# Performance work log

Measured on AMD Instinct MI355X. Metric: run time of the kernel, lower is better.

Reference implementation:

```python
import jax, jax.numpy as jnp
import numpy as np

PATCH = 9  # patch_size
EPS = 1e-12  # F.normalize eps


def _l2norm(x, axis):
    n = jnp.sqrt(jnp.sum(x * x, axis=axis, keepdims=True))
    return x / jnp.maximum(n, EPS)


def setup_inputs() -> dict:
    key = jax.random.key(0)
    k1, k2, k3 = jax.random.split(key, 3)
    feat_tar = jax.random.normal(k1, (16384, 512), dtype=jnp.float32)
    feat_refs = jax.random.normal(k2, (8, 512, 16384), dtype=jnp.float32)
    label_refs = jax.random.uniform(k3, (8, 32, 128, 128), dtype=jnp.float32)
    return {"feat_tar": feat_tar, "feat_refs": feat_refs, "label_refs": label_refs}


def reference(feat_tar, feat_refs, label_refs):
    num_ctx, num_labels, h, w = label_refs.shape
    num_feats = feat_tar.shape[1]
    P, pad = PATCH, PATCH // 2

    # feature_normalization=True: L2-normalize along feature dim
    feat_tar = _l2norm(feat_tar, axis=1)           # [h*w, C]
    feat_refs = _l2norm(feat_refs, axis=1)         # [nc, C, h*w]

    tar = feat_tar.T.reshape(num_feats, h, w)      # [C, h, w]
    refs = feat_refs.reshape(num_ctx, num_feats, h, w)
    refs_pad = jnp.pad(refs, ((0, 0), (0, 0), (pad, pad), (pad, pad)))

    # local correlation: corr[b, dy*P+dx, y, x] = sum_c refs_pad[b,c,y+dy,x+dx] * tar[c,y,x]
    # (matches F.unfold(refs, P, padding=pad) * tar -> sum over c)
    rows = []
    for dy in range(P):
        for dx in range(P):
            win = jax.lax.dynamic_slice(
                refs_pad, (0, 0, dy, dx), (num_ctx, num_feats, h, w))
            rows.append(jnp.einsum('bchw,chw->bhw', win, tar))
    corr = jnp.stack(rows, axis=1)                 # [nc, P*P, h, w]

    aff = corr.reshape(num_ctx, P * P, h * w).transpose(0, 2, 1)  # [nc, h*w, P*P]

    # affinity_normalization = Softmax(dim=-1)
    return jax.nn.softmax(aff, axis=-1)
```

## Files before the change

### kernel.cpp

```cpp
#include <hip/hip_runtime.h>
#include <hip/hip_bf16.h>

#define HW 128
#define NPIX 16384
#define CDEP 512
#define NB 8
#define QT 32

typedef __attribute__((ext_vector_type(8))) short short8;
typedef __attribute__((ext_vector_type(8))) __bf16 bf16x8;
typedef __attribute__((ext_vector_type(4))) float f32x4;

static __device__ inline bf16x8 asbf(short8 v) {
  union { short8 s; bf16x8 b; } u; u.s = v; return u.b;
}

static __device__ inline unsigned short f2bf(float x) {
  unsigned u = __float_as_uint(x);
  unsigned r = (u + 0x7fffu + ((u >> 16) & 1u)) >> 16;
  return (unsigned short)r;
}

__global__ __launch_bounds__(256) void k_norm_tar(const float* __restrict__ ft,
                                                  unsigned short* __restrict__ T) {
  int wave = threadIdx.x >> 6, lane = threadIdx.x & 63;
  int p = blockIdx.x * 4 + wave;
  const float* row = ft + (size_t)p * CDEP + lane * 8;
  float4 v0 = *(const float4*)(row);
  float4 v1 = *(const float4*)(row + 4);
  float s = v0.x*v0.x + v0.y*v0.y + v0.z*v0.z + v0.w*v0.w
          + v1.x*v1.x + v1.y*v1.y + v1.z*v1.z + v1.w*v1.w;
  #pragma unroll
  for (int off = 1; off < 64; off <<= 1) s += __shfl_xor(s, off);
  float sc = 1.0f / fmaxf(sqrtf(s), 1e-12f);
  float vv[8] = {v0.x, v0.y, v0.z, v0.w, v1.x, v1.y, v1.z, v1.w};
  short8 pk;
  #pragma unroll
  for (int i = 0; i < 8; ++i) pk[i] = (short)f2bf(vv[i] * sc);
  *(short8*)(T + (size_t)p * CDEP + lane * 8) = pk;
}

__global__ __launch_bounds__(256) void k_norm_refs(const float* __restrict__ fr,
                                                   unsigned short* __restrict__ R,
                                                   int b_offset) {
  __shared__ float lds[QT][CDEP + 1];
  __shared__ float psum[QT][8];
  __shared__ float inv[QT];
  int b = b_offset + blockIdx.z;
  int q0 = blockIdx.x * QT;
  const float* src = fr + (size_t)b * CDEP * NPIX;
  int t = threadIdx.x;

  int g = t & 7, cy = t >> 3;
  #pragma unroll
  for (int it = 0; it < 16; ++it) {
    int c = it * 32 + cy;
    float4 v = *(const float4*)(src + (size_t)c * NPIX + q0 + g * 4);
    lds[g*4 + 0][c] = v.x;
    lds[g*4 + 1][c] = v.y;
    lds[g*4 + 2][c] = v.z;
    lds[g*4 + 3][c] = v.w;
  }
  __syncthreads();

  int p = t & 31, part = t >> 5;
  float s = 0.f;
  #pragma unroll
  for (int j = 0; j < 64; ++j) { float v = lds[p][part*64 + j]; s += v * v; }
  psum[p][part] = s;
  __syncthreads();
  if (t < QT) {
    float a = 0.f;
    #pragma unroll
    for (int j = 0; j < 8; ++j) a += psum[t][j];
    inv[t] = 1.0f / fmaxf(sqrtf(a), 1e-12f);
  }
  __syncthreads();

  unsigned short* dst = R + ((size_t)blockIdx.z * NPIX + q0) * CDEP;
  #pragma unroll 4
  for (int j = 0; j < QT; ++j) {
    float sc = inv[j];
    unsigned lo = f2bf(lds[j][2*t]     * sc);
    unsigned hi = f2bf(lds[j][2*t + 1] * sc);
    *(unsigned*)(dst + (size_t)j * CDEP + 2*t) = lo | (hi << 16);
  }
}

__global__ __launch_bounds__(256, 2) void k_corr(const unsigned short* __restrict__ Tb,
                                                 const unsigned short* __restrict__ Rall,
                                                 float* __restrict__ out,
                                                 int b_offset) {
  __shared__ __align__(16) unsigned char ldsb[65536];
  const int t = threadIdx.x;
  const int lane = t & 63, wave = t >> 6;
  const int wy = wave >> 1, wx = wave & 1;
  const int bx = blockIdx.x, by = blockIdx.y, bz = blockIdx.z;
  const int b = b_offset + bz;
  const short* Rb = (const short*)Rall + (size_t)bz * NPIX * CDEP;
  const short* Tp = (const short*)Tb;

  const int mA = lane & 15, kg = lane >> 4;
  const int py = by*8 + wy*4 + (mA >> 2), px = bx*8 + wx*4 + (mA & 3);
  const short* arow = Tp + (size_t)(py * HW + px) * CDEP + kg * 8;
  short8 a[16];
  #pragma unroll
  for (int kk = 0; kk < 16; ++kk) a[kk] = *(const short8*)(arow + kk * 32);

  const int slot = t & 7, qbase = t >> 3;
  int goff[8]; unsigned gval = 0; int loff[8];
  #pragma unroll
  for (int r = 0; r < 8; ++r) {
    int q = r * 32 + qbase;
    int gy = by*8 - 4 + (q >> 4);
    int gx = bx*8 - 4 + (q & 15);
    bool v = ((unsigned)gy < (unsigned)HW) && ((unsigned)gx < (unsigned)HW);
    if (v) gval |= (1u << r);
    goff[r] = v ? ((gy * HW + gx) * CDEP + slot * 8) : 0;
    loff[r] = q * 128 + ((slot * 16) ^ ((q & 7) << 4));
  }

  int qn[9];
  #pragma unroll
  for (int tt = 0; tt < 9; ++tt) {
    int idx = tt * 16 + (lane & 15);
    int qly = wy*4 + idx / 12, qlx = wx*4 + idx % 12;
    qn[tt] = qly * 16 + qlx;
  }

  f32x4 acc[9];
  #pragma unroll
  for (int tt = 0; tt < 9; ++tt) acc[tt] = (f32x4){0.f, 0.f, 0.f, 0.f};

  short8 st[8];
  const short8 z8 = {0,0,0,0,0,0,0,0};

  #pragma unroll
  for (int r = 0; r < 8; ++r)
    st[r] = ((gval >> r) & 1) ? *(const short8*)(Rb + goff[r]) : z8;
  #pragma unroll
  for (int r = 0; r < 8; ++r)
    *(short8*)(ldsb + loff[r]) = st[r];
  __syncthreads();

  #pragma unroll
  for (int ch = 0; ch < 8; ++ch) {
    if (ch < 7) {
      const short* src = Rb + (ch + 1) * 64;
      #pragma unroll
      for (int r = 0; r < 8; ++r)
        st[r] = ((gval >> r) & 1) ? *(const short8*)(src + goff[r]) : z8;
    }
    const int bufb = (ch & 1) << 15;
    #pragma unroll
    for (int step = 0; step < 2; ++step) {
      short8 af = a[ch * 2 + step];
      #pragma unroll
      for (int tt = 0; tt < 9; ++tt) {
        int q = qn[tt];
        int off = bufb + q * 128 + (((step << 6) | (kg << 4)) ^ ((q & 7) << 4));
        short8 bf = *(const short8*)(ldsb + off);
        acc[tt] = __builtin_amdgcn_mfma_f32_16x16x32_bf16(asbf(af), asbf(bf), acc[tt], 0, 0, 0);
      }
    }
    if (ch < 7) {
      const int nbuf = ((ch + 1) & 1) << 15;
      #pragma unroll
      for (int r = 0; r < 8; ++r)
        *(short8*)(ldsb + nbuf + loff[r]) = st[r];
      __syncthreads();
    }
  }

  __syncthreads();

  const int SSTR = 148;
  float* S = (float*)ldsb + wave * 16 * SSTR;
  #pragma unroll
  for (int tt = 0; tt < 9; ++tt) {
    #pragma unroll
    for (int r = 0; r < 4; ++r)
      S[(kg * 4 + r) * SSTR + tt * 16 + (lane & 15)] = acc[tt][r];
  }
  __syncthreads();

  const int mrow = lane >> 2, s4 = lane & 3;
  const int myy = mrow >> 2, mxx = mrow & 3;
  const float* Srow = S + mrow * SSTR;
  float vals[21];
  float mx = -3.0e38f;
  #pragma unroll
  for (int i = 0; i < 21; ++i) {
    int j = s4 + 4 * i;
    if (j < 81) {
      int dy = j / 9, dx = j % 9;
      float v = Srow[(myy + dy) * 12 + (mxx + dx)];
      vals[i] = v;
      mx = fmaxf(mx, v);
    }
  }
  mx = fmaxf(mx, __shfl_xor(mx, 1));
  mx = fmaxf(mx, __shfl_xor(mx, 2));
  float sum = 0.f;
  #pragma unroll
  for (int i = 0; i < 21; ++i) {
    int j = s4 + 4 * i;
    if (j < 81) { float e = __expf(vals[i] - mx); vals[i] = e; sum += e; }
  }
  sum += __shfl_xor(sum, 1);
  sum += __shfl_xor(sum, 2);
  float rs = 1.0f / sum;
  const int pg = (by*8 + wy*4 + myy) * HW + (bx*8 + wx*4 + mxx);
  float* op = out + ((size_t)b * NPIX + pg) * 81;
  #pragma unroll
  for (int i = 0; i < 21; ++i) {
    int j = s4 + 4 * i;
    if (j < 81) op[j] = vals[i] * rs;
  }
}

extern "C" void kernel_launch(void* const* d_in, const int* in_sizes, int n_in,
                              void* d_out, int out_size, void* d_ws, size_t ws_size,
                              hipStream_t stream) {
  const float* ft = (const float*)d_in[0];
  const float* fr = (const float*)d_in[1];
  float* out = (float*)d_out;
  unsigned short* T = (unsigned short*)d_ws;
  unsigned short* R = T + (size_t)NPIX * CDEP;
  size_t needAll = ((size_t)NPIX * CDEP + (size_t)NB * NPIX * CDEP) * 2;

  k_norm_tar<<<dim3(NPIX / 4), dim3(256), 0, stream>>>(ft, T);
  if (ws_size >= needAll) {
    k_norm_refs<<<dim3(NPIX / QT, 1, NB), dim3(256), 0, stream>>>(fr, R, 0);
    k_corr<<<dim3(16, 16, NB), dim3(256), 0, stream>>>(T, R, out, 0);
  } else {
    for (int bb = 0; bb < NB; ++bb) {
      k_norm_refs<<<dim3(NPIX / QT, 1, 1), dim3(256), 0, stream>>>(fr, R, bb);
      k_corr<<<dim3(16, 16, 1), dim3(256), 0, stream>>>(T, R, out, bb);
    }
  }
}
```

Measured before the change: 161.0 us.

## Stream reference tiles into LDS via global_load_lds with pre-swizzled layout

```diff
diff --git a/kernel.cpp b/kernel.cpp
--- a/kernel.cpp
+++ b/kernel.cpp
@@ -5,7 +5,6 @@
 #define NPIX 16384
 #define CDEP 512
 #define NB 8
-#define QT 32
 
 typedef __attribute__((ext_vector_type(8))) short short8;
 typedef __attribute__((ext_vector_type(8))) __bf16 bf16x8;
@@ -14,15 +13,24 @@
 static __device__ inline bf16x8 asbf(short8 v) {
   union { short8 s; bf16x8 b; } u; u.s = v; return u.b;
 }
-
 static __device__ inline unsigned short f2bf(float x) {
   unsigned u = __float_as_uint(x);
-  unsigned r = (u + 0x7fffu + ((u >> 16) & 1u)) >> 16;
-  return (unsigned short)r;
+  return (unsigned short)((u + 0x7fffu + ((u >> 16) & 1u)) >> 16);
+}
+static __device__ inline unsigned pk2(float lo, float hi) {
+  return (unsigned)f2bf(lo) | ((unsigned)f2bf(hi) << 16);
+}
+static __device__ inline void gload16(const void* g, void* l) {
+  __builtin_amdgcn_global_load_lds(
+      (const __attribute__((address_space(1))) unsigned int*)g,
+      (__attribute__((address_space(3))) unsigned int*)l, 16, 0, 0);
 }
 
 __global__ __launch_bounds__(256) void k_norm_tar(const float* __restrict__ ft,
-                                                  unsigned short* __restrict__ T) {
+                                                  unsigned short* __restrict__ T,
+                                                  float* __restrict__ zp) {
+  if (blockIdx.x == 0 && threadIdx.x < 64)
+    ((f32x4*)zp)[threadIdx.x] = (f32x4){0.f, 0.f, 0.f, 0.f};
   int wave = threadIdx.x >> 6, lane = threadIdx.x & 63;
   int p = blockIdx.x * 4 + wave;
   const float* row = ft + (size_t)p * CDEP + lane * 8;
@@ -34,20 +42,20 @@
   for (int off = 1; off < 64; off <<= 1) s += __shfl_xor(s, off);
   float sc = 1.0f / fmaxf(sqrtf(s), 1e-12f);
   float vv[8] = {v0.x, v0.y, v0.z, v0.w, v1.x, v1.y, v1.z, v1.w};
-  short8 pk;
-  #pragma unroll
-  for (int i = 0; i < 8; ++i) pk[i] = (short)f2bf(vv[i] * sc);
-  *(short8*)(T + (size_t)p * CDEP + lane * 8) = pk;
+  short8 pkv;
+  #pragma unroll
+  for (int i = 0; i < 8; ++i) pkv[i] = (short)f2bf(vv[i] * sc);
+  *(short8*)(T + (size_t)p * CDEP + lane * 8) = pkv;
 }
 
 __global__ __launch_bounds__(256) void k_norm_refs(const float* __restrict__ fr,
                                                    unsigned short* __restrict__ R,
                                                    int b_offset) {
-  __shared__ float lds[QT][CDEP + 1];
-  __shared__ float psum[QT][8];
-  __shared__ float inv[QT];
+  __shared__ float lds[32][CDEP + 1];
+  __shared__ float psum[32][8];
+  __shared__ float inv[32];
   int b = b_offset + blockIdx.z;
-  int q0 = blockIdx.x * QT;
+  int q0 = blockIdx.x * 32;
   const float* src = fr + (size_t)b * CDEP * NPIX;
   int t = threadIdx.x;
 
@@ -69,7 +77,7 @@
   for (int j = 0; j < 64; ++j) { float v = lds[p][part*64 + j]; s += v * v; }
   psum[p][part] = s;
   __syncthreads();
-  if (t < QT) {
+  if (t < 32) {
     float a = 0.f;
     #pragma unroll
     for (int j = 0; j < 8; ++j) a += psum[t][j];
@@ -77,110 +85,97 @@
   }
   __syncthreads();
 
-  unsigned short* dst = R + ((size_t)blockIdx.z * NPIX + q0) * CDEP;
+  unsigned char* dstb = (unsigned char*)(R + (size_t)blockIdx.z * NPIX * CDEP);
+  const int chunk = t >> 5, sl = (t & 31) >> 2, w4 = (t & 3) * 4;
   #pragma unroll 4
-  for (int j = 0; j < QT; ++j) {
+  for (int j = 0; j < 32; ++j) {
+    int pg = q0 + j;
+    int key = (pg + 4) & 7;
+    int off = chunk * 128 + ((sl ^ key) << 4) + w4;
     float sc = inv[j];
-    unsigned lo = f2bf(lds[j][2*t]     * sc);
-    unsigned hi = f2bf(lds[j][2*t + 1] * sc);
-    *(unsigned*)(dst + (size_t)j * CDEP + 2*t) = lo | (hi << 16);
+    *(unsigned*)(dstb + (size_t)pg * 1024 + off) = pk2(lds[j][2*t] * sc, lds[j][2*t + 1] * sc);
   }
 }
 
 __global__ __launch_bounds__(256, 2) void k_corr(const unsigned short* __restrict__ Tb,
-                                                 const unsigned short* __restrict__ Rall,
+                                                 const unsigned short* __restrict__ R,
+                                                 const float* __restrict__ zp,
                                                  float* __restrict__ out,
-                                                 int b_offset) {
-  __shared__ __align__(16) unsigned char ldsb[65536];
-  const int t = threadIdx.x;
-  const int lane = t & 63, wave = t >> 6;
+                                                 int b_offset, int shift) {
+  __shared__ __align__(16) unsigned char lds[65536];
+  const int t = threadIdx.x, lane = t & 63, wave = t >> 6;
+  const int lb = blockIdx.x;
+  const int logical = (lb & 7) * (1 << shift) + (lb >> 3);
+  const int bx = logical & 15, by = (logical >> 4) & 15, bz = logical >> 8;
   const int wy = wave >> 1, wx = wave & 1;
-  const int bx = blockIdx.x, by = blockIdx.y, bz = blockIdx.z;
-  const int b = b_offset + bz;
-  const short* Rb = (const short*)Rall + (size_t)bz * NPIX * CDEP;
-  const short* Tp = (const short*)Tb;
-
   const int mA = lane & 15, kg = lane >> 4;
-  const int py = by*8 + wy*4 + (mA >> 2), px = bx*8 + wx*4 + (mA & 3);
-  const short* arow = Tp + (size_t)(py * HW + px) * CDEP + kg * 8;
+  const unsigned char* Rb = (const unsigned char*)(R + (size_t)bz * NPIX * CDEP);
+
+  const unsigned char* ptr8[8];
+  #pragma unroll
+  for (int r = 0; r < 8; ++r) {
+    int q = r * 32 + wave * 8 + (lane >> 3);
+    int gy = by * 8 - 4 + (q >> 4), gx = bx * 8 - 4 + (q & 15);
+    bool valid = ((unsigned)gy < 128u) && ((unsigned)gx < 128u);
+    const unsigned char* base = valid ? (Rb + (size_t)(gy * HW + gx) * 1024)
+                                      : (const unsigned char*)zp;
+    ptr8[r] = base + (lane & 7) * 16;
+  }
+
+  int qoff[9];
+  #pragma unroll
+  for (int tt = 0; tt < 9; ++tt) {
+    int idx = tt * 16 + mA;
+    int q = (wy * 4 + idx / 12) * 16 + (wx * 4 + idx % 12);
+    qoff[tt] = q * 128 + ((kg << 4) ^ ((q & 7) << 4));
+  }
+
+  const int py = by * 8 + wy * 4 + (mA >> 2), px = bx * 8 + wx * 4 + (mA & 3);
+  const short* arow = (const short*)Tb + (size_t)(py * HW + px) * CDEP + kg * 8;
   short8 a[16];
   #pragma unroll
   for (int kk = 0; kk < 16; ++kk) a[kk] = *(const short8*)(arow + kk * 32);
 
-  const int slot = t & 7, qbase = t >> 3;
-  int goff[8]; unsigned gval = 0; int loff[8];
-  #pragma unroll
-  for (int r = 0; r < 8; ++r) {
-    int q = r * 32 + qbase;
-    int gy = by*8 - 4 + (q >> 4);
-    int gx = bx*8 - 4 + (q & 15);
-    bool v = ((unsigned)gy < (unsigned)HW) && ((unsigned)gx < (unsigned)HW);
-    if (v) gval |= (1u << r);
-    goff[r] = v ? ((gy * HW + gx) * CDEP + slot * 8) : 0;
-    loff[r] = q * 128 + ((slot * 16) ^ ((q & 7) << 4));
-  }
-
-  int qn[9];
-  #pragma unroll
-  for (int tt = 0; tt < 9; ++tt) {
-    int idx = tt * 16 + (lane & 15);
-    int qly = wy*4 + idx / 12, qlx = wx*4 + idx % 12;
-    qn[tt] = qly * 16 + qlx;
-  }
-
   f32x4 acc[9];
   #pragma unroll
   for (int tt = 0; tt < 9; ++tt) acc[tt] = (f32x4){0.f, 0.f, 0.f, 0.f};
 
-  short8 st[8];
-  const short8 z8 = {0,0,0,0,0,0,0,0};
-
   #pragma unroll
   for (int r = 0; r < 8; ++r)
-    st[r] = ((gval >> r) & 1) ? *(const short8*)(Rb + goff[r]) : z8;
-  #pragma unroll
-  for (int r = 0; r < 8; ++r)
-    *(short8*)(ldsb + loff[r]) = st[r];
+    gload16(ptr8[r], lds + r * 4096 + wave * 1024);
   __syncthreads();
 
   #pragma unroll
   for (int ch = 0; ch < 8; ++ch) {
     if (ch < 7) {
-      const short* src = Rb + (ch + 1) * 64;
+      const int nb = ((ch + 1) & 1) << 15;
       #pragma unroll
       for (int r = 0; r < 8; ++r)
-        st[r] = ((gval >> r) & 1) ? *(const short8*)(src + goff[r]) : z8;
-    }
-    const int bufb = (ch & 1) << 15;
+        gload16(ptr8[r] + (ch + 1) * 128, lds + nb + r * 4096 + wave * 1024);
+    }
+    const int bufo = (ch & 1) << 15;
+    __builtin_amdgcn_s_setprio(1);
     #pragma unroll
     for (int step = 0; step < 2; ++step) {
-      short8 af = a[ch * 2 + step];
+      bf16x8 af = asbf(a[ch * 2 + step]);
+      const int sx = step << 6;
       #pragma unroll
       for (int tt = 0; tt < 9; ++tt) {
-        int q = qn[tt];
-        int off = bufb + q * 128 + (((step << 6) | (kg << 4)) ^ ((q & 7) << 4));
-        short8 bf = *(const short8*)(ldsb + off);
-        acc[tt] = __builtin_amdgcn_mfma_f32_16x16x32_bf16(asbf(af), asbf(bf), acc[tt], 0, 0, 0);
+        short8 bv = *(const short8*)(lds + bufo + (qoff[tt] ^ sx));
+        acc[tt] = __builtin_amdgcn_mfma_f32_16x16x32_bf16(af, asbf(bv), acc[tt], 0, 0, 0);
       }
     }
-    if (ch < 7) {
-      const int nbuf = ((ch + 1) & 1) << 15;
-      #pragma unroll
-      for (int r = 0; r < 8; ++r)
-        *(short8*)(ldsb + nbuf + loff[r]) = st[r];
-      __syncthreads();
-    }
-  }
-
-  __syncthreads();
+    __builtin_amdgcn_s_setprio(0);
+    __syncthreads();
+  }
 
   const int SSTR = 148;
-  float* S = (float*)ldsb + wave * 16 * SSTR;
+  float* S = (float*)lds + wave * 16 * SSTR;
   #pragma unroll
   for (int tt = 0; tt < 9; ++tt) {
     #pragma unroll
     for (int r = 0; r < 4; ++r)
-      S[(kg * 4 + r) * SSTR + tt * 16 + (lane & 15)] = acc[tt][r];
+      S[(kg * 4 + r) * SSTR + tt * 16 + mA] = acc[tt][r];
   }
   __syncthreads();
 
@@ -210,8 +205,8 @@
   sum += __shfl_xor(sum, 1);
   sum += __shfl_xor(sum, 2);
   float rs = 1.0f / sum;
-  const int pg = (by*8 + wy*4 + myy) * HW + (bx*8 + wx*4 + mxx);
-  float* op = out + ((size_t)b * NPIX + pg) * 81;
+  const int pg = (by * 8 + wy * 4 + myy) * HW + (bx * 8 + wx * 4 + mxx);
+  float* op = out + ((size_t)(b_offset + bz) * NPIX + pg) * 81;
   #pragma unroll
   for (int i = 0; i < 21; ++i) {
     int j = s4 + 4 * i;
@@ -225,18 +220,24 @@
   const float* ft = (const float*)d_in[0];
   const float* fr = (const float*)d_in[1];
   float* out = (float*)d_out;
+
+  const size_t T_BYTES = (size_t)NPIX * CDEP * 2;
+  const size_t ZP_OFF  = T_BYTES;
+  const size_t R_OFF   = T_BYTES + 4096;
+  const size_t R_FULL  = (size_t)NB * NPIX * CDEP * 2;
+
   unsigned short* T = (unsigned short*)d_ws;
-  unsigned short* R = T + (size_t)NPIX * CDEP;
-  size_t needAll = ((size_t)NPIX * CDEP + (size_t)NB * NPIX * CDEP) * 2;
-
-  k_norm_tar<<<dim3(NPIX / 4), dim3(256), 0, stream>>>(ft, T);
-  if (ws_size >= needAll) {
-    k_norm_refs<<<dim3(NPIX / QT, 1, NB), dim3(256), 0, stream>>>(fr, R, 0);
-    k_corr<<<dim3(16, 16, NB), dim3(256), 0, stream>>>(T, R, out, 0);
+  float* zp = (float*)((char*)d_ws + ZP_OFF);
+  unsigned short* R = (unsigned short*)((char*)d_ws + R_OFF);
+
+  k_norm_tar<<<dim3(NPIX / 4), dim3(256), 0, stream>>>(ft, T, zp);
+  if (ws_size >= R_OFF + R_FULL) {
+    k_norm_refs<<<dim3(512, 1, NB), dim3(256), 0, stream>>>(fr, R, 0);
+    k_corr<<<dim3(2048), dim3(256), 0, stream>>>(T, R, zp, out, 0, 8);
   } else {
     for (int bb = 0; bb < NB; ++bb) {
-      k_norm_refs<<<dim3(NPIX / QT, 1, 1), dim3(256), 0, stream>>>(fr, R, bb);
-      k_corr<<<dim3(16, 16, 1), dim3(256), 0, stream>>>(T, R, out, bb);
-    }
-  }
-}
+      k_norm_refs<<<dim3(512, 1, 1), dim3(256), 0, stream>>>(fr, R, bb);
+      k_corr<<<dim3(256), dim3(256), 0, stream>>>(T, R, zp, out, bb, 5);
+    }
+  }
+}
```

Result: slower. 165.9 us (+3.0%).
